# Optimization experiments

Hardware: AMD Instinct MI355X
Metric: run time of the kernel (lower is better)

## Reference

```python
import jax, jax.numpy as jnp
import numpy as np

HEAD_SIZE = 64
N_EMBD = 768

def setup_inputs() -> dict:
    key = jax.random.key(0)
    kx, kq, kk, kv = jax.random.split(key, 4)
    x = jax.random.normal(kx, (4, 4096, N_EMBD), dtype=jnp.float32)
    s = 1.0 / np.sqrt(N_EMBD)
    Wq = jax.random.normal(kq, (N_EMBD, HEAD_SIZE), dtype=jnp.float32) * s
    Wk = jax.random.normal(kk, (N_EMBD, HEAD_SIZE), dtype=jnp.float32) * s
    Wv = jax.random.normal(kv, (N_EMBD, HEAD_SIZE), dtype=jnp.float32) * s
    return {"x": x, "Wq": Wq, "Wk": Wk, "Wv": Wv}

def reference(x, Wq, Wk, Wv):
    b, t, c = x.shape
    h = Wq.shape[1]
    q = jnp.einsum('btc,ch->bth', x, Wq)
    k = jnp.einsum('btc,ch->bth', x, Wk)
    v = jnp.einsum('btc,ch->bth', x, Wv)
    scores = jnp.einsum('bqh,bkh->bqk', q, k) / jnp.sqrt(jnp.float32(h))
    causal = jnp.tril(jnp.ones((t, t), dtype=bool))  # [t,t]
    scores = jnp.where(causal, scores, -jnp.inf)
    attn = jax.nn.softmax(scores, axis=-1)
    return jnp.einsum('bqk,bkh->bqh', attn, v)
```

## Files before the change

### kernel.cpp

```cpp
#include <hip/hip_runtime.h>
#include <math.h>

#define BB 4
#define TT 4096
#define CC 768
#define HH 64
#define NN 192
#define LDP 72
#define GR 32
#define BKK 64

typedef __bf16 bf16x8 __attribute__((ext_vector_type(8)));
typedef float floatx4 __attribute__((ext_vector_type(4)));
typedef unsigned short u16x8 __attribute__((ext_vector_type(8)));

__device__ inline unsigned short f2bf(float f) {
    union { __bf16 b; unsigned short u; } v;
    v.b = (__bf16)f;
    return v.u;
}

__global__ __launch_bounds__(256) void wprep(const float* __restrict__ Wq,
                                             const float* __restrict__ Wk,
                                             const float* __restrict__ Wv,
                                             unsigned short* __restrict__ wt) {
    const int idx = blockIdx.x * 256 + threadIdx.x;
    if (idx >= NN * CC) return;
    const int n = idx / CC, c = idx - n * CC;
    const float* W = (n < 64) ? Wq : (n < 128) ? Wk : Wv;
    wt[idx] = f2bf(W[c * HH + (n & 63)]);
}

__global__ __launch_bounds__(256) void qkv_gemm(const float* __restrict__ x,
                                                const unsigned short* __restrict__ wt,
                                                unsigned short* __restrict__ qb,
                                                unsigned short* __restrict__ kb,
                                                unsigned short* __restrict__ vbt) {
    __shared__ unsigned short As[GR * LDP];
    __shared__ unsigned short Bs[NN * LDP];

    const int tid = threadIdx.x;
    const int w = tid >> 6, lane = tid & 63;
    const int l15 = lane & 15, quad = lane >> 4;
    const int m0 = blockIdx.x * GR;
    const int r0 = (w & 1) * 16;
    const int n0 = (w >> 1) * 96;

    floatx4 acc[6] = {};

    for (int k0 = 0; k0 < CC; k0 += BKK) {
        __syncthreads();
#pragma unroll
        for (int e = 0; e < 2; ++e) {
            const int c = tid + 256 * e;
            const int r = c >> 4, c4 = (c & 15) * 4;
            const float4 v = *(const float4*)(x + (size_t)(m0 + r) * CC + k0 + c4);
            ushort4 pk;
            pk.x = f2bf(v.x); pk.y = f2bf(v.y); pk.z = f2bf(v.z); pk.w = f2bf(v.w);
            *(ushort4*)(As + r * LDP + c4) = pk;
        }
#pragma unroll
        for (int e = 0; e < 6; ++e) {
            const int c = tid + 256 * e;
            const int r = c >> 3, c8 = (c & 7) * 8;
            *(u16x8*)(Bs + r * LDP + c8) = *(const u16x8*)(wt + (size_t)r * CC + k0 + c8);
        }
        __syncthreads();

        const bf16x8 a0 = *(const bf16x8*)(As + (r0 + l15) * LDP + quad * 8);
        const bf16x8 a1 = *(const bf16x8*)(As + (r0 + l15) * LDP + 32 + quad * 8);
#pragma unroll
        for (int j = 0; j < 6; ++j) {
            const bf16x8 b0 = *(const bf16x8*)(Bs + (n0 + j * 16 + l15) * LDP + quad * 8);
            const bf16x8 b1 = *(const bf16x8*)(Bs + (n0 + j * 16 + l15) * LDP + 32 + quad * 8);
            acc[j] = __builtin_amdgcn_mfma_f32_16x16x32_bf16(a0, b0, acc[j], 0, 0, 0);
            acc[j] = __builtin_amdgcn_mfma_f32_16x16x32_bf16(a1, b1, acc[j], 0, 0, 0);
        }
    }

    const int b = m0 >> 12;
    const int tloc = (m0 & (TT - 1)) + r0 + quad * 4;
#pragma unroll
    for (int j = 0; j < 6; ++j) {
        const int n = n0 + j * 16 + l15;
        const int mid = n >> 6;
        const int h = n & 63;
        if (mid == 2) {
            ushort4 pk;
            pk.x = f2bf(acc[j][0]); pk.y = f2bf(acc[j][1]);
            pk.z = f2bf(acc[j][2]); pk.w = f2bf(acc[j][3]);
            *(ushort4*)(vbt + ((size_t)b * HH + h) * TT + tloc) = pk;
        } else {
            unsigned short* dst = (mid == 0) ? qb : kb;
#pragma unroll
            for (int r = 0; r < 4; ++r)
                dst[(size_t)(m0 + r0 + quad * 4 + r) * HH + h] = f2bf(acc[j][r]);
        }
    }
}

__global__ __launch_bounds__(256) void attn_part(const unsigned short* __restrict__ qb,
                                                 const unsigned short* __restrict__ kb,
                                                 const unsigned short* __restrict__ vbt,
                                                 float* __restrict__ Opart,
                                                 float* __restrict__ ml) {
    __shared__ unsigned short Ks[64 * LDP];
    __shared__ unsigned short VTs[64 * LDP];
    __shared__ unsigned short Ps[4][16 * LDP];

    const int b   = blockIdx.x / 160;
    const int rem = blockIdx.x - b * 160;
    int qt, ch;
    if (rem < 16)      { qt = rem;               ch = 0; }
    else if (rem < 48) { qt = 16 + (rem - 16) / 2; ch = (rem - 16) % 2; }
    else if (rem < 96) { qt = 32 + (rem - 48) / 3; ch = (rem - 48) % 3; }
    else               { qt = 48 + (rem - 96) / 4; ch = (rem - 96) % 4; }

    const int q0  = qt * 64;
    const int tid = threadIdx.x;
    const int w = tid >> 6, lane = tid & 63;
    const int l15 = lane & 15, quad = lane >> 4;

    const unsigned short* Qb  = qb  + (size_t)b * TT * HH;
    const unsigned short* Kb  = kb  + (size_t)b * TT * HH;
    const unsigned short* VTb = vbt + (size_t)b * HH * TT;

    const int qrow = q0 + 16 * w + l15;
    const bf16x8 qf0 = *(const bf16x8*)(Qb + (size_t)qrow * HH + quad * 8);
    const bf16x8 qf1 = *(const bf16x8*)(Qb + (size_t)qrow * HH + 32 + quad * 8);

    floatx4 O[4] = {};
    float m_r[4], l_r[4];
#pragma unroll
    for (int r = 0; r < 4; ++r) { m_r[r] = -INFINITY; l_r[r] = 0.f; }

    const int kt0 = ch * 16;
    const int kt1 = min(kt0 + 16, qt + 1);
    for (int kt = kt0; kt < kt1; ++kt) {
        __syncthreads();
        const unsigned short* Kt = Kb + (size_t)(kt * 64) * HH;
        const unsigned short* Vt = VTb + kt * 64;
#pragma unroll
        for (int e = 0; e < 2; ++e) {
            const int chunk = tid + 256 * e;
            const int r = chunk >> 3, c0 = (chunk & 7) * 8;
            *(u16x8*)(Ks + r * LDP + c0)  = *(const u16x8*)(Kt + r * HH + c0);
            *(u16x8*)(VTs + r * LDP + c0) = *(const u16x8*)(Vt + (size_t)r * TT + c0);
        }
        __syncthreads();

        floatx4 s[4];
#pragma unroll
        for (int ki = 0; ki < 4; ++ki) {
            const bf16x8 kf0 = *(const bf16x8*)(Ks + (16 * ki + l15) * LDP + quad * 8);
            const bf16x8 kf1 = *(const bf16x8*)(Ks + (16 * ki + l15) * LDP + 32 + quad * 8);
            floatx4 c = {};
            c = __builtin_amdgcn_mfma_f32_16x16x32_bf16(qf0, kf0, c, 0, 0, 0);
            c = __builtin_amdgcn_mfma_f32_16x16x32_bf16(qf1, kf1, c, 0, 0, 0);
            s[ki] = c * 0.125f;
        }

        if (kt == qt) {
#pragma unroll
            for (int ki = 0; ki < 4; ++ki)
#pragma unroll
                for (int r = 0; r < 4; ++r) {
                    const int kloc = 16 * ki + l15;
                    const int qloc = 16 * w + quad * 4 + r;
                    if (kloc > qloc) s[ki][r] = -INFINITY;
                }
        }

        float mx[4], alpha[4], rs[4];
#pragma unroll
        for (int r = 0; r < 4; ++r) {
            float v = fmaxf(fmaxf(s[0][r], s[1][r]), fmaxf(s[2][r], s[3][r]));
#pragma unroll
            for (int msk = 8; msk >= 1; msk >>= 1) v = fmaxf(v, __shfl_xor(v, msk, 64));
            mx[r] = fmaxf(v, m_r[r]);
            alpha[r] = __expf(m_r[r] - mx[r]);
            rs[r] = 0.f;
        }
#pragma unroll
        for (int ki = 0; ki < 4; ++ki)
#pragma unroll
            for (int r = 0; r < 4; ++r) {
                const float p = __expf(s[ki][r] - mx[r]);
                s[ki][r] = p;
                rs[r] += p;
            }
#pragma unroll
        for (int r = 0; r < 4; ++r) {
            float v = rs[r];
#pragma unroll
            for (int msk = 8; msk >= 1; msk >>= 1) v += __shfl_xor(v, msk, 64);
            l_r[r] = l_r[r] * alpha[r] + v;
            m_r[r] = mx[r];
        }
#pragma unroll
        for (int di = 0; di < 4; ++di)
#pragma unroll
            for (int r = 0; r < 4; ++r) O[di][r] *= alpha[r];

        unsigned short* Pw = Ps[w];
#pragma unroll
        for (int ki = 0; ki < 4; ++ki)
#pragma unroll
            for (int r = 0; r < 4; ++r)
                Pw[(quad * 4 + r) * LDP + 16 * ki + l15] = f2bf(s[ki][r]);

        const bf16x8 pf0 = *(const bf16x8*)(Pw + l15 * LDP + quad * 8);
        const bf16x8 pf1 = *(const bf16x8*)(Pw + l15 * LDP + 32 + quad * 8);
#pragma unroll
        for (int di = 0; di < 4; ++di) {
            const bf16x8 vf0 = *(const bf16x8*)(VTs + (16 * di + l15) * LDP + quad * 8);
            const bf16x8 vf1 = *(const bf16x8*)(VTs + (16 * di + l15) * LDP + 32 + quad * 8);
            O[di] = __builtin_amdgcn_mfma_f32_16x16x32_bf16(pf0, vf0, O[di], 0, 0, 0);
            O[di] = __builtin_amdgcn_mfma_f32_16x16x32_bf16(pf1, vf1, O[di], 0, 0, 0);
        }
    }

    const int pbase = ((b * 64 + qt) * 4 + ch) * 64;
    float* Op = Opart + (size_t)pbase * HH + 16 * w * HH;
#pragma unroll
    for (int di = 0; di < 4; ++di)
#pragma unroll
        for (int r = 0; r < 4; ++r)
            Op[(quad * 4 + r) * HH + 16 * di + l15] = O[di][r];
    if (l15 == 0) {
#pragma unroll
        for (int r = 0; r < 4; ++r) {
            const int prow = pbase + 16 * w + quad * 4 + r;
            ml[prow * 2]     = m_r[r];
            ml[prow * 2 + 1] = l_r[r];
        }
    }
}

__global__ __launch_bounds__(256) void attn_merge(const float* __restrict__ Opart,
                                                  const float* __restrict__ ml,
                                                  float* __restrict__ out) {
    const int g = blockIdx.x * 256 + threadIdx.x;
    const int row = g >> 6, d = g & 63;
    const int b = row >> 12, t = row & (TT - 1);
    const int qt = t >> 6, rloc = t & 63;
    const int nchunk = (qt >> 4) + 1;
    const int pbase = ((b * 64 + qt) * 4) * 64 + rloc;

    float M = -INFINITY;
#pragma unroll 4
    for (int c = 0; c < nchunk; ++c) M = fmaxf(M, ml[(pbase + c * 64) * 2]);
    float O = 0.f, L = 0.f;
#pragma unroll 4
    for (int c = 0; c < nchunk; ++c) {
        const int idx = pbase + c * 64;
        const float wgt = __expf(ml[idx * 2] - M);
        L += wgt * ml[idx * 2 + 1];
        O += wgt * Opart[(size_t)idx * HH + d];
    }
    out[(size_t)row * HH + d] = O / L;
}

__global__ __launch_bounds__(256) void attn_full(const unsigned short* __restrict__ qb,
                                                 const unsigned short* __restrict__ kb,
                                                 const unsigned short* __restrict__ vbt,
                                                 float* __restrict__ out) {
    __shared__ unsigned short Ks[64 * LDP];
    __shared__ unsigned short VTs[64 * LDP];
    __shared__ unsigned short Ps[4][16 * LDP];

    const int b   = blockIdx.x >> 6;
    const int qt  = blockIdx.x & 63;
    const int q0  = qt * 64;
    const int tid = threadIdx.x;
    const int w = tid >> 6, lane = tid & 63;
    const int l15 = lane & 15, quad = lane >> 4;

    const unsigned short* Qb  = qb  + (size_t)b * TT * HH;
    const unsigned short* Kb  = kb  + (size_t)b * TT * HH;
    const unsigned short* VTb = vbt + (size_t)b * HH * TT;

    const int qrow = q0 + 16 * w + l15;
    const bf16x8 qf0 = *(const bf16x8*)(Qb + (size_t)qrow * HH + quad * 8);
    const bf16x8 qf1 = *(const bf16x8*)(Qb + (size_t)qrow * HH + 32 + quad * 8);

    floatx4 O[4] = {};
    float m_r[4], l_r[4];
#pragma unroll
    for (int r = 0; r < 4; ++r) { m_r[r] = -INFINITY; l_r[r] = 0.f; }

    for (int kt = 0; kt <= qt; ++kt) {
        __syncthreads();
        const unsigned short* Kt = Kb + (size_t)(kt * 64) * HH;
        const unsigned short* Vt = VTb + kt * 64;
#pragma unroll
        for (int e = 0; e < 2; ++e) {
            const int chunk = tid + 256 * e;
            const int r = chunk >> 3, c0 = (chunk & 7) * 8;
            *(u16x8*)(Ks + r * LDP + c0)  = *(const u16x8*)(Kt + r * HH + c0);
            *(u16x8*)(VTs + r * LDP + c0) = *(const u16x8*)(Vt + (size_t)r * TT + c0);
        }
        __syncthreads();

        floatx4 s[4];
#pragma unroll
        for (int ki = 0; ki < 4; ++ki) {
            const bf16x8 kf0 = *(const bf16x8*)(Ks + (16 * ki + l15) * LDP + quad * 8);
            const bf16x8 kf1 = *(const bf16x8*)(Ks + (16 * ki + l15) * LDP + 32 + quad * 8);
            floatx4 c = {};
            c = __builtin_amdgcn_mfma_f32_16x16x32_bf16(qf0, kf0, c, 0, 0, 0);
            c = __builtin_amdgcn_mfma_f32_16x16x32_bf16(qf1, kf1, c, 0, 0, 0);
            s[ki] = c * 0.125f;
        }
        if (kt == qt) {
#pragma unroll
            for (int ki = 0; ki < 4; ++ki)
#pragma unroll
                for (int r = 0; r < 4; ++r)
                    if (16 * ki + l15 > 16 * w + quad * 4 + r) s[ki][r] = -INFINITY;
        }
        float mx[4], alpha[4], rs[4];
#pragma unroll
        for (int r = 0; r < 4; ++r) {
            float v = fmaxf(fmaxf(s[0][r], s[1][r]), fmaxf(s[2][r], s[3][r]));
#pragma unroll
            for (int msk = 8; msk >= 1; msk >>= 1) v = fmaxf(v, __shfl_xor(v, msk, 64));
            mx[r] = fmaxf(v, m_r[r]);
            alpha[r] = __expf(m_r[r] - mx[r]);
            rs[r] = 0.f;
        }
#pragma unroll
        for (int ki = 0; ki < 4; ++ki)
#pragma unroll
            for (int r = 0; r < 4; ++r) {
                const float p = __expf(s[ki][r] - mx[r]);
                s[ki][r] = p; rs[r] += p;
            }
#pragma unroll
        for (int r = 0; r < 4; ++r) {
            float v = rs[r];
#pragma unroll
            for (int msk = 8; msk >= 1; msk >>= 1) v += __shfl_xor(v, msk, 64);
            l_r[r] = l_r[r] * alpha[r] + v;
            m_r[r] = mx[r];
        }
#pragma unroll
        for (int di = 0; di < 4; ++di)
#pragma unroll
            for (int r = 0; r < 4; ++r) O[di][r] *= alpha[r];

        unsigned short* Pw = Ps[w];
#pragma unroll
        for (int ki = 0; ki < 4; ++ki)
#pragma unroll
            for (int r = 0; r < 4; ++r)
                Pw[(quad * 4 + r) * LDP + 16 * ki + l15] = f2bf(s[ki][r]);

        const bf16x8 pf0 = *(const bf16x8*)(Pw + l15 * LDP + quad * 8);
        const bf16x8 pf1 = *(const bf16x8*)(Pw + l15 * LDP + 32 + quad * 8);
#pragma unroll
        for (int di = 0; di < 4; ++di) {
            const bf16x8 vf0 = *(const bf16x8*)(VTs + (16 * di + l15) * LDP + quad * 8);
            const bf16x8 vf1 = *(const bf16x8*)(VTs + (16 * di + l15) * LDP + 32 + quad * 8);
            O[di] = __builtin_amdgcn_mfma_f32_16x16x32_bf16(pf0, vf0, O[di], 0, 0, 0);
            O[di] = __builtin_amdgcn_mfma_f32_16x16x32_bf16(pf1, vf1, O[di], 0, 0, 0);
        }
    }
    float* outp = out + ((size_t)b * TT + q0 + 16 * w) * HH;
#pragma unroll
    for (int di = 0; di < 4; ++di)
#pragma unroll
        for (int r = 0; r < 4; ++r)
            outp[(quad * 4 + r) * HH + 16 * di + l15] = O[di][r] / l_r[r];
}

extern "C" void kernel_launch(void* const* d_in, const int* in_sizes, int n_in,
                              void* d_out, int out_size, void* d_ws, size_t ws_size,
                              hipStream_t stream) {
    const float* x  = (const float*)d_in[0];
    const float* Wq = (const float*)d_in[1];
    const float* Wk = (const float*)d_in[2];
    const float* Wv = (const float*)d_in[3];
    float* out = (float*)d_out;

    const size_t nQKV = (size_t)BB * TT * HH;
    unsigned short* qb  = (unsigned short*)d_ws;
    unsigned short* kb  = qb + nQKV;
    unsigned short* vbt = kb + nQKV;
    unsigned short* wt  = vbt + nQKV;
    char* after_wt = (char*)(wt + (size_t)NN * CC);
    float* Opart = (float*)after_wt;
    float* ml    = Opart + (size_t)256 * 4 * 64 * HH;
    const size_t need = (size_t)((char*)(ml + 256 * 4 * 64 * 2) - (char*)d_ws);

    wprep<<<(NN * CC + 255) / 256, 256, 0, stream>>>(Wq, Wk, Wv, wt);
    qkv_gemm<<<(BB * TT) / GR, 256, 0, stream>>>(x, wt, qb, kb, vbt);
    if (ws_size >= need) {
        attn_part<<<BB * 160, 256, 0, stream>>>(qb, kb, vbt, Opart, ml);
        attn_merge<<<(BB * TT * HH) / 256, 256, 0, stream>>>(Opart, ml, out);
    } else {
        attn_full<<<BB * (TT / 64), 256, 0, stream>>>(qb, kb, vbt, out);
    }
}
```

Measured before the change: 155.8 us.

## Load K/V fragments directly from global in attention; retile QKV GEMM warps

In both attention kernels, the cooperative LDS staging of K and V^T tiles and both __syncthreads per key tile are removed. Each wave now loads its MFMA operand fragments straight from global memory and depends on L1/L2 caching for reuse across the four waves. Separately, the QKV GEMM gives each wave all 32 rows and 48 columns instead of 16 rows and 96 columns, so each B fragment feeds two MFMAs. The attention change trades barrier and LDS traffic for four times the global/L2 load traffic and possibly more exposed latency.

```diff
diff --git a/kernel.cpp b/kernel.cpp
--- a/kernel.cpp
+++ b/kernel.cpp
@@ -43,10 +43,9 @@
     const int w = tid >> 6, lane = tid & 63;
     const int l15 = lane & 15, quad = lane >> 4;
     const int m0 = blockIdx.x * GR;
-    const int r0 = (w & 1) * 16;
-    const int n0 = (w >> 1) * 96;
-
-    floatx4 acc[6] = {};
+    const int n0 = w * 48;
+
+    floatx4 acc[2][3] = {};
 
     for (int k0 = 0; k0 < CC; k0 += BKK) {
         __syncthreads();
@@ -67,34 +66,44 @@
         }
         __syncthreads();
 
-        const bf16x8 a0 = *(const bf16x8*)(As + (r0 + l15) * LDP + quad * 8);
-        const bf16x8 a1 = *(const bf16x8*)(As + (r0 + l15) * LDP + 32 + quad * 8);
-#pragma unroll
-        for (int j = 0; j < 6; ++j) {
+        bf16x8 a0[2], a1[2];
+#pragma unroll
+        for (int rg = 0; rg < 2; ++rg) {
+            a0[rg] = *(const bf16x8*)(As + (16 * rg + l15) * LDP + quad * 8);
+            a1[rg] = *(const bf16x8*)(As + (16 * rg + l15) * LDP + 32 + quad * 8);
+        }
+#pragma unroll
+        for (int j = 0; j < 3; ++j) {
             const bf16x8 b0 = *(const bf16x8*)(Bs + (n0 + j * 16 + l15) * LDP + quad * 8);
             const bf16x8 b1 = *(const bf16x8*)(Bs + (n0 + j * 16 + l15) * LDP + 32 + quad * 8);
-            acc[j] = __builtin_amdgcn_mfma_f32_16x16x32_bf16(a0, b0, acc[j], 0, 0, 0);
-            acc[j] = __builtin_amdgcn_mfma_f32_16x16x32_bf16(a1, b1, acc[j], 0, 0, 0);
+#pragma unroll
+            for (int rg = 0; rg < 2; ++rg) {
+                acc[rg][j] = __builtin_amdgcn_mfma_f32_16x16x32_bf16(a0[rg], b0, acc[rg][j], 0, 0, 0);
+                acc[rg][j] = __builtin_amdgcn_mfma_f32_16x16x32_bf16(a1[rg], b1, acc[rg][j], 0, 0, 0);
+            }
         }
     }
 
     const int b = m0 >> 12;
-    const int tloc = (m0 & (TT - 1)) + r0 + quad * 4;
-#pragma unroll
-    for (int j = 0; j < 6; ++j) {
+#pragma unroll
+    for (int j = 0; j < 3; ++j) {
         const int n = n0 + j * 16 + l15;
         const int mid = n >> 6;
         const int h = n & 63;
-        if (mid == 2) {
-            ushort4 pk;
-            pk.x = f2bf(acc[j][0]); pk.y = f2bf(acc[j][1]);
-            pk.z = f2bf(acc[j][2]); pk.w = f2bf(acc[j][3]);
-            *(ushort4*)(vbt + ((size_t)b * HH + h) * TT + tloc) = pk;
-        } else {
-            unsigned short* dst = (mid == 0) ? qb : kb;
-#pragma unroll
-            for (int r = 0; r < 4; ++r)
-                dst[(size_t)(m0 + r0 + quad * 4 + r) * HH + h] = f2bf(acc[j][r]);
+#pragma unroll
+        for (int rg = 0; rg < 2; ++rg) {
+            const int tloc = (m0 & (TT - 1)) + 16 * rg + quad * 4;
+            if (mid == 2) {
+                ushort4 pk;
+                pk.x = f2bf(acc[rg][j][0]); pk.y = f2bf(acc[rg][j][1]);
+                pk.z = f2bf(acc[rg][j][2]); pk.w = f2bf(acc[rg][j][3]);
+                *(ushort4*)(vbt + ((size_t)b * HH + h) * TT + tloc) = pk;
+            } else {
+                unsigned short* dst = (mid == 0) ? qb : kb;
+#pragma unroll
+                for (int r = 0; r < 4; ++r)
+                    dst[(size_t)(m0 + 16 * rg + quad * 4 + r) * HH + h] = f2bf(acc[rg][j][r]);
+            }
         }
     }
 }
@@ -104,8 +113,6 @@
                                                  const unsigned short* __restrict__ vbt,
                                                  float* __restrict__ Opart,
                                                  float* __restrict__ ml) {
-    __shared__ unsigned short Ks[64 * LDP];
-    __shared__ unsigned short VTs[64 * LDP];
     __shared__ unsigned short Ps[4][16 * LDP];
 
     const int b   = blockIdx.x / 160;
@@ -137,23 +144,14 @@
     const int kt0 = ch * 16;
     const int kt1 = min(kt0 + 16, qt + 1);
     for (int kt = kt0; kt < kt1; ++kt) {
-        __syncthreads();
         const unsigned short* Kt = Kb + (size_t)(kt * 64) * HH;
-        const unsigned short* Vt = VTb + kt * 64;
-#pragma unroll
-        for (int e = 0; e < 2; ++e) {
-            const int chunk = tid + 256 * e;
-            const int r = chunk >> 3, c0 = (chunk & 7) * 8;
-            *(u16x8*)(Ks + r * LDP + c0)  = *(const u16x8*)(Kt + r * HH + c0);
-            *(u16x8*)(VTs + r * LDP + c0) = *(const u16x8*)(Vt + (size_t)r * TT + c0);
-        }
-        __syncthreads();
 
         floatx4 s[4];
 #pragma unroll
         for (int ki = 0; ki < 4; ++ki) {
-            const bf16x8 kf0 = *(const bf16x8*)(Ks + (16 * ki + l15) * LDP + quad * 8);
-            const bf16x8 kf1 = *(const bf16x8*)(Ks + (16 * ki + l15) * LDP + 32 + quad * 8);
+            const unsigned short* Kr = Kt + (size_t)(16 * ki + l15) * HH + quad * 8;
+            const bf16x8 kf0 = *(const bf16x8*)(Kr);
+            const bf16x8 kf1 = *(const bf16x8*)(Kr + 32);
             floatx4 c = {};
             c = __builtin_amdgcn_mfma_f32_16x16x32_bf16(qf0, kf0, c, 0, 0, 0);
             c = __builtin_amdgcn_mfma_f32_16x16x32_bf16(qf1, kf1, c, 0, 0, 0);
@@ -213,8 +211,9 @@
         const bf16x8 pf1 = *(const bf16x8*)(Pw + l15 * LDP + 32 + quad * 8);
 #pragma unroll
         for (int di = 0; di < 4; ++di) {
-            const bf16x8 vf0 = *(const bf16x8*)(VTs + (16 * di + l15) * LDP + quad * 8);
-            const bf16x8 vf1 = *(const bf16x8*)(VTs + (16 * di + l15) * LDP + 32 + quad * 8);
+            const unsigned short* Vr = VTb + (size_t)(16 * di + l15) * TT + kt * 64 + quad * 8;
+            const bf16x8 vf0 = *(const bf16x8*)(Vr);
+            const bf16x8 vf1 = *(const bf16x8*)(Vr + 32);
             O[di] = __builtin_amdgcn_mfma_f32_16x16x32_bf16(pf0, vf0, O[di], 0, 0, 0);
             O[di] = __builtin_amdgcn_mfma_f32_16x16x32_bf16(pf1, vf1, O[di], 0, 0, 0);
         }
@@ -265,8 +264,6 @@
                                                  const unsigned short* __restrict__ kb,
                                                  const unsigned short* __restrict__ vbt,
                                                  float* __restrict__ out) {
-    __shared__ unsigned short Ks[64 * LDP];
-    __shared__ unsigned short VTs[64 * LDP];
     __shared__ unsigned short Ps[4][16 * LDP];
 
     const int b   = blockIdx.x >> 6;
@@ -290,23 +287,13 @@
     for (int r = 0; r < 4; ++r) { m_r[r] = -INFINITY; l_r[r] = 0.f; }
 
     for (int kt = 0; kt <= qt; ++kt) {
-        __syncthreads();
         const unsigned short* Kt = Kb + (size_t)(kt * 64) * HH;
-        const unsigned short* Vt = VTb + kt * 64;
-#pragma unroll
-        for (int e = 0; e < 2; ++e) {
-            const int chunk = tid + 256 * e;
-            const int r = chunk >> 3, c0 = (chunk & 7) * 8;
-            *(u16x8*)(Ks + r * LDP + c0)  = *(const u16x8*)(Kt + r * HH + c0);
-            *(u16x8*)(VTs + r * LDP + c0) = *(const u16x8*)(Vt + (size_t)r * TT + c0);
-        }
-        __syncthreads();
-
         floatx4 s[4];
 #pragma unroll
         for (int ki = 0; ki < 4; ++ki) {
-            const bf16x8 kf0 = *(const bf16x8*)(Ks + (16 * ki + l15) * LDP + quad * 8);
-            const bf16x8 kf1 = *(const bf16x8*)(Ks + (16 * ki + l15) * LDP + 32 + quad * 8);
+            const unsigned short* Kr = Kt + (size_t)(16 * ki + l15) * HH + quad * 8;
+            const bf16x8 kf0 = *(const bf16x8*)(Kr);
+            const bf16x8 kf1 = *(const bf16x8*)(Kr + 32);
             floatx4 c = {};
             c = __builtin_amdgcn_mfma_f32_16x16x32_bf16(qf0, kf0, c, 0, 0, 0);
             c = __builtin_amdgcn_mfma_f32_16x16x32_bf16(qf1, kf1, c, 0, 0, 0);
@@ -360,8 +347,9 @@
         const bf16x8 pf1 = *(const bf16x8*)(Pw + l15 * LDP + 32 + quad * 8);
 #pragma unroll
         for (int di = 0; di < 4; ++di) {
-            const bf16x8 vf0 = *(const bf16x8*)(VTs + (16 * di + l15) * LDP + quad * 8);
-            const bf16x8 vf1 = *(const bf16x8*)(VTs + (16 * di + l15) * LDP + 32 + quad * 8);
+            const unsigned short* Vr = VTb + (size_t)(16 * di + l15) * TT + kt * 64 + quad * 8;
+            const bf16x8 vf0 = *(const bf16x8*)(Vr);
+            const bf16x8 vf1 = *(const bf16x8*)(Vr + 32);
             O[di] = __builtin_amdgcn_mfma_f32_16x16x32_bf16(pf0, vf0, O[di], 0, 0, 0);
             O[di] = __builtin_amdgcn_mfma_f32_16x16x32_bf16(pf1, vf1, O[di], 0, 0, 0);
         }
```

Result: slower. 194.4 us (+24.7%).
